# Kernel tuning notes

Hardware: AMD Instinct MI355X
Metric: run time of the kernel (lower is better)

## Reference

```python
import jax, jax.numpy as jnp
import numpy as np

B, N, L, D, O = 64, 4096, 64, 512, 7
K = 10  # topk neighbors per ligand atom (k=10 in pool_lig)
EPS_BN = 1e-5


def setup_inputs() -> dict:
    key = jax.random.key(0)
    ks = jax.random.split(key, 6)
    pos = jax.random.normal(ks[0], (B, N, 3), jnp.float32) * 10.0
    x = jax.random.normal(ks[1], (B, N, D), jnp.float32)
    lig_coords = jax.random.normal(ks[2], (B, L, 3), jnp.float32) * 10.0
    W1 = jax.random.normal(ks[3], (D, D), jnp.float32) / np.sqrt(D).astype(np.float32)
    b1 = jnp.zeros((D,), jnp.float32)
    gamma = jnp.ones((D,), jnp.float32)
    beta = jnp.zeros((D,), jnp.float32)
    W2 = jax.random.normal(ks[4], (O, D), jnp.float32) / np.sqrt(D).astype(np.float32)
    b2 = jnp.zeros((O,), jnp.float32)
    return dict(pos=pos, x=x, lig_coords=lig_coords, W1=W1, b1=b1,
                gamma=gamma, beta=beta, W2=W2, b2=b2)


def _pool_lig(pos_b, x_b, lig_b):
    # cdist: [N, L] pairwise euclidean distances
    d = jnp.sqrt(jnp.sum((pos_b[:, None, :] - lig_b[None, :, :]) ** 2, axis=-1))
    # topk(-d, k=K, dim=0): K nearest surface points per ligand atom -> [L, K]
    idx = jax.lax.top_k(-d.T, K)[1]
    # .unique() + gather + mean == mean over the set of unique selected rows.
    # Implement via a 0/1 membership mask (scatter-set dedups repeats).
    mask = jnp.zeros((pos_b.shape[0],), x_b.dtype).at[idx.reshape(-1)].set(1.0)
    return (mask[:, None] * x_b).sum(axis=0) / mask.sum()  # [D]


def reference(pos, x, lig_coords, W1, b1, gamma, beta, W2, b2):
    emb = jax.vmap(_pool_lig)(pos, x, lig_coords)  # [B, D]
    h = emb @ W1.T + b1                             # Linear(D, D)
    # Dropout(p=0.1): identity (eval / deterministic reference)
    mu = h.mean(axis=0)
    var = h.var(axis=0)  # biased variance, as BatchNorm1d (training stats)
    h = gamma * (h - mu) / jnp.sqrt(var + EPS_BN) + beta
    h = h * jax.nn.sigmoid(h)                       # SiLU
    return h @ W2.T + b2                            # [B, O]
```

## Files before the change

kernel.cpp:

```cpp
#include <hip/hip_runtime.h>

#define BATCH 64
#define NPTS  4096
#define LIG   64
#define DIM   512
#define OUTF  7
#define TOPK  10

using ull = unsigned long long;

__device__ __forceinline__ ull shfl_down_u64(ull v, int off) {
    unsigned int lo = (unsigned int)v, hi = (unsigned int)(v >> 32);
    lo = __shfl_down(lo, off);
    hi = __shfl_down(hi, off);
    return ((ull)hi << 32) | lo;
}

__device__ __forceinline__ float dot4(float4 a, float4 b) {
    return a.x * b.x + a.y * b.y + a.z * b.z + a.w * b.w;
}

__global__ __launch_bounds__(256) void k_topk(
    const float* __restrict__ pos,
    const float* __restrict__ lig,
    int* __restrict__ idxbuf) {
    const int l = blockIdx.x;
    const int b = blockIdx.y;
    const int t = threadIdx.x;

    const float* lp = lig + ((size_t)b * LIG + l) * 3;
    const float lx = lp[0], ly = lp[1], lz = lp[2];

    const float4* src = (const float4*)(pos + (size_t)b * NPTS * 3) + t * 12;
    float w[48];
#pragma unroll
    for (int q = 0; q < 12; ++q) {
        float4 v = src[q];
        w[4 * q] = v.x; w[4 * q + 1] = v.y; w[4 * q + 2] = v.z; w[4 * q + 3] = v.w;
    }

    ull key[16];
#pragma unroll
    for (int i = 0; i < 16; ++i) {
        float dx = w[3 * i]     - lx;
        float dy = w[3 * i + 1] - ly;
        float dz = w[3 * i + 2] - lz;
        float d2 = dx * dx + dy * dy + dz * dz;
        key[i] = ((ull)__float_as_uint(d2) << 32) | (unsigned)(t * 16 + i);
    }

    __shared__ ull red[4];
    __shared__ unsigned int widx_sh;
    const int wave = t >> 6, lane = t & 63;

    for (int r = 0; r < TOPK; ++r) {
        ull k = key[0];
#pragma unroll
        for (int i = 1; i < 16; ++i) k = (key[i] < k) ? key[i] : k;
#pragma unroll
        for (int off = 32; off > 0; off >>= 1) {
            ull o = shfl_down_u64(k, off);
            k = (o < k) ? o : k;
        }
        if (lane == 0) red[wave] = k;
        __syncthreads();
        if (t == 0) {
            ull m = red[0];
#pragma unroll
            for (int i = 1; i < 4; ++i) m = (red[i] < m) ? red[i] : m;
            unsigned int widx = (unsigned int)m;
            widx_sh = widx;
            idxbuf[((size_t)b * LIG + l) * TOPK + r] = (int)widx;
        }
        __syncthreads();
        const unsigned int widx = widx_sh;
#pragma unroll
        for (int i = 0; i < 16; ++i)
            if (widx == (unsigned)(t * 16 + i)) key[i] = ~0ull;
    }
}

__global__ __launch_bounds__(256) void k_pool(
    const int* __restrict__ idxbuf,
    const float* __restrict__ x,
    float* __restrict__ emb) {
    const int c = blockIdx.x;
    const int b = blockIdx.y;
    const int t = threadIdx.x;

    __shared__ unsigned mword[NPTS / 32];
    __shared__ int list[LIG * TOPK];
    __shared__ int cnt;
    if (t == 0) cnt = 0;
    for (int i = t; i < NPTS / 32; i += 256) mword[i] = 0u;
    __syncthreads();

    const int* ib = idxbuf + (size_t)b * LIG * TOPK;
    for (int j = t; j < LIG * TOPK; j += 256) {
        int idx = ib[j];
        unsigned bit = 1u << (idx & 31);
        unsigned old = atomicOr(&mword[idx >> 5], bit);
        if (!(old & bit)) list[atomicAdd(&cnt, 1)] = idx;
    }
    __syncthreads();
    const int n_sel = cnt;
    const float inv = 1.0f / (float)n_sel;

    const float* xb = x + (size_t)b * NPTS * DIM + c * 256 + t;
    float a = 0.f;
    int j = 0;
    for (; j + 4 <= n_sel; j += 4) {
        int n0 = list[j], n1 = list[j + 1], n2 = list[j + 2], n3 = list[j + 3];
        float v0 = xb[(size_t)n0 * DIM];
        float v1 = xb[(size_t)n1 * DIM];
        float v2 = xb[(size_t)n2 * DIM];
        float v3 = xb[(size_t)n3 * DIM];
        a += v0 + v1 + v2 + v3;
    }
    for (; j < n_sel; ++j) a += xb[(size_t)list[j] * DIM];

    emb[(size_t)b * DIM + c * 256 + t] = a * inv;
}

__global__ __launch_bounds__(256) void k_fc1(
    const float* __restrict__ emb,
    const float* __restrict__ W1,
    const float* __restrict__ b1,
    float* __restrict__ h) {
    const int jc = blockIdx.x;
    const int b  = blockIdx.y;
    const int t  = threadIdx.x;
    const int wave = t >> 6, lane = t & 63;

    const float4* ep = (const float4*)(emb + (size_t)b * DIM) + lane * 2;
    float4 e0 = ep[0], e1 = ep[1];

#pragma unroll
    for (int q = 0; q < 16; ++q) {
        const int jj = jc * 64 + wave * 16 + q;
        const float4* wp = (const float4*)(W1 + (size_t)jj * DIM) + lane * 2;
        float s = dot4(wp[0], e0) + dot4(wp[1], e1);
#pragma unroll
        for (int off = 32; off > 0; off >>= 1) s += __shfl_down(s, off);
        if (lane == 0) h[(size_t)b * DIM + jj] = s + b1[jj];
    }
}

__global__ __launch_bounds__(512) void k_bn(
    const float* __restrict__ h,
    const float* __restrict__ gamma,
    const float* __restrict__ beta,
    float* __restrict__ hs) {
    const int jf = threadIdx.x;
    float s = 0.f, ss = 0.f;
#pragma unroll 8
    for (int b = 0; b < BATCH; ++b) {
        float v = h[(size_t)b * DIM + jf];
        s += v; ss += v * v;
    }
    const float mu  = s * (1.0f / BATCH);
    const float var = ss * (1.0f / BATCH) - mu * mu;
    const float inv = rsqrtf(var + 1e-5f);
    const float g  = gamma[jf];
    const float be = beta[jf];
#pragma unroll 8
    for (int b = 0; b < BATCH; ++b) {
        float v = h[(size_t)b * DIM + jf];
        float u = g * (v - mu) * inv + be;
        hs[(size_t)b * DIM + jf] = u / (1.0f + __expf(-u));
    }
}

__global__ __launch_bounds__(64) void k_fc2(
    const float* __restrict__ hs,
    const float* __restrict__ W2,
    const float* __restrict__ b2,
    float* __restrict__ out) {
    const int b = blockIdx.x;
    const int lane = threadIdx.x;
    const float4* hp = (const float4*)(hs + (size_t)b * DIM) + lane * 2;
    float4 h0 = hp[0], h1 = hp[1];
#pragma unroll
    for (int o = 0; o < OUTF; ++o) {
        const float4* wp = (const float4*)(W2 + (size_t)o * DIM) + lane * 2;
        float s = dot4(wp[0], h0) + dot4(wp[1], h1);
#pragma unroll
        for (int off = 32; off > 0; off >>= 1) s += __shfl_down(s, off);
        if (lane == 0) out[(size_t)b * OUTF + o] = s + b2[o];
    }
}

extern "C" void kernel_launch(void* const* d_in, const int* in_sizes, int n_in,
                              void* d_out, int out_size, void* d_ws, size_t ws_size,
                              hipStream_t stream) {
    const float* pos   = (const float*)d_in[0];
    const float* x     = (const float*)d_in[1];
    const float* lig   = (const float*)d_in[2];
    const float* W1    = (const float*)d_in[3];
    const float* b1    = (const float*)d_in[4];
    const float* gamma = (const float*)d_in[5];
    const float* beta  = (const float*)d_in[6];
    const float* W2    = (const float*)d_in[7];
    const float* b2    = (const float*)d_in[8];
    float* out = (float*)d_out;

    char* ws = (char*)d_ws;
    int*   idxbuf = (int*)ws;
    float* emb    = (float*)(ws + (size_t)BATCH * LIG * TOPK * 4);
    float* h      = emb + BATCH * DIM;
    float* hs     = h + BATCH * DIM;

    k_topk<<<dim3(LIG, BATCH), 256, 0, stream>>>(pos, lig, idxbuf);
    k_pool<<<dim3(2, BATCH), 256, 0, stream>>>(idxbuf, x, emb);
    k_fc1 <<<dim3(8, BATCH), 256, 0, stream>>>(emb, W1, b1, h);
    k_bn  <<<1, 512, 0, stream>>>(h, gamma, beta, hs);
    k_fc2 <<<BATCH, 64, 0, stream>>>(hs, W2, b2, out);
}
```

Measured before the change: 687.0 us.

## Split pooling gather across row-partition blocks and cache per-thread min in top-k

The pooling kernel now partitions the selected rows by index modulo 8 across 8 blocks per batch, not splitting columns across 2 blocks. Each block writes partial sums, and fc1 reduces them and divides by a popcount-based unique count. This raises parallelism for the latency-bound gather at the cost of extra partial traffic and a dedup pass repeated in every block. The top-k loop caches each thread's minimum and recomputes it only in the thread that owns the winner, and it uses double-buffered shared slots so one barrier per round suffices.

```diff
diff --git a/kernel.cpp b/kernel.cpp
--- a/kernel.cpp
+++ b/kernel.cpp
@@ -6,6 +6,7 @@
 #define DIM   512
 #define OUTF  7
 #define TOPK  10
+#define PBLK  8
 
 using ull = unsigned long long;
 
@@ -15,6 +16,8 @@
     hi = __shfl_down(hi, off);
     return ((ull)hi << 32) | lo;
 }
+
+__device__ __forceinline__ ull umin64(ull a, ull b) { return (a < b) ? a : b; }
 
 __device__ __forceinline__ float dot4(float4 a, float4 b) {
     return a.x * b.x + a.y * b.y + a.z * b.z + a.w * b.w;
@@ -49,49 +52,50 @@
         key[i] = ((ull)__float_as_uint(d2) << 32) | (unsigned)(t * 16 + i);
     }
 
-    __shared__ ull red[4];
-    __shared__ unsigned int widx_sh;
+    ull m = key[0];
+#pragma unroll
+    for (int i = 1; i < 16; ++i) m = umin64(m, key[i]);
+
+    __shared__ ull red[2][4];
     const int wave = t >> 6, lane = t & 63;
+    int* ob = idxbuf + ((size_t)b * LIG + l) * TOPK;
 
     for (int r = 0; r < TOPK; ++r) {
-        ull k = key[0];
-#pragma unroll
-        for (int i = 1; i < 16; ++i) k = (key[i] < k) ? key[i] : k;
-#pragma unroll
-        for (int off = 32; off > 0; off >>= 1) {
-            ull o = shfl_down_u64(k, off);
-            k = (o < k) ? o : k;
+        ull k = m;
+#pragma unroll
+        for (int off = 32; off > 0; off >>= 1)
+            k = umin64(k, shfl_down_u64(k, off));
+        if (lane == 0) red[r & 1][wave] = k;
+        __syncthreads();
+        const ull g = umin64(umin64(red[r & 1][0], red[r & 1][1]),
+                             umin64(red[r & 1][2], red[r & 1][3]));
+        const unsigned widx = (unsigned)g;
+        if (t == 0) ob[r] = (int)widx;
+        if ((widx >> 4) == (unsigned)t) {
+#pragma unroll
+            for (int i = 0; i < 16; ++i)
+                key[i] = (key[i] == g) ? ~0ull : key[i];
+            m = key[0];
+#pragma unroll
+            for (int i = 1; i < 16; ++i) m = umin64(m, key[i]);
         }
-        if (lane == 0) red[wave] = k;
-        __syncthreads();
-        if (t == 0) {
-            ull m = red[0];
-#pragma unroll
-            for (int i = 1; i < 4; ++i) m = (red[i] < m) ? red[i] : m;
-            unsigned int widx = (unsigned int)m;
-            widx_sh = widx;
-            idxbuf[((size_t)b * LIG + l) * TOPK + r] = (int)widx;
-        }
-        __syncthreads();
-        const unsigned int widx = widx_sh;
-#pragma unroll
-        for (int i = 0; i < 16; ++i)
-            if (widx == (unsigned)(t * 16 + i)) key[i] = ~0ull;
     }
 }
 
 __global__ __launch_bounds__(256) void k_pool(
     const int* __restrict__ idxbuf,
     const float* __restrict__ x,
-    float* __restrict__ emb) {
-    const int c = blockIdx.x;
+    float* __restrict__ partial,
+    int* __restrict__ nsel) {
+    const int p = blockIdx.x;
     const int b = blockIdx.y;
     const int t = threadIdx.x;
 
     __shared__ unsigned mword[NPTS / 32];
     __shared__ int list[LIG * TOPK];
     __shared__ int cnt;
-    if (t == 0) cnt = 0;
+    __shared__ int tot;
+    if (t == 0) { cnt = 0; tot = 0; }
     for (int i = t; i < NPTS / 32; i += 256) mword[i] = 0u;
     __syncthreads();
 
@@ -100,30 +104,47 @@
         int idx = ib[j];
         unsigned bit = 1u << (idx & 31);
         unsigned old = atomicOr(&mword[idx >> 5], bit);
-        if (!(old & bit)) list[atomicAdd(&cnt, 1)] = idx;
+        if (!(old & bit) && ((idx & 7) == p)) list[atomicAdd(&cnt, 1)] = idx;
     }
     __syncthreads();
-    const int n_sel = cnt;
-    const float inv = 1.0f / (float)n_sel;
-
-    const float* xb = x + (size_t)b * NPTS * DIM + c * 256 + t;
-    float a = 0.f;
+
+    int v = (t < NPTS / 32) ? (int)__popc(mword[t]) : 0;
+#pragma unroll
+    for (int off = 32; off > 0; off >>= 1) v += __shfl_down(v, off);
+    if ((t & 63) == 0) atomicAdd(&tot, v);
+    __syncthreads();
+    if (p == 0 && t == 0) nsel[b] = tot;
+
+    const int cn = cnt;
+    const float* xb = x + (size_t)b * NPTS * DIM + t;
+    float a0 = 0.f, a1 = 0.f;
     int j = 0;
-    for (; j + 4 <= n_sel; j += 4) {
+    for (; j + 3 < cn; j += 4) {
         int n0 = list[j], n1 = list[j + 1], n2 = list[j + 2], n3 = list[j + 3];
-        float v0 = xb[(size_t)n0 * DIM];
-        float v1 = xb[(size_t)n1 * DIM];
-        float v2 = xb[(size_t)n2 * DIM];
-        float v3 = xb[(size_t)n3 * DIM];
-        a += v0 + v1 + v2 + v3;
-    }
-    for (; j < n_sel; ++j) a += xb[(size_t)list[j] * DIM];
-
-    emb[(size_t)b * DIM + c * 256 + t] = a * inv;
+        const float* r0 = xb + (size_t)n0 * DIM;
+        const float* r1 = xb + (size_t)n1 * DIM;
+        const float* r2 = xb + (size_t)n2 * DIM;
+        const float* r3 = xb + (size_t)n3 * DIM;
+        float v00 = r0[0], v01 = r0[256];
+        float v10 = r1[0], v11 = r1[256];
+        float v20 = r2[0], v21 = r2[256];
+        float v30 = r3[0], v31 = r3[256];
+        a0 += v00 + v10 + v20 + v30;
+        a1 += v01 + v11 + v21 + v31;
+    }
+    for (; j < cn; ++j) {
+        const float* r0 = xb + (size_t)list[j] * DIM;
+        a0 += r0[0]; a1 += r0[256];
+    }
+
+    float* pb = partial + ((size_t)b * PBLK + p) * DIM;
+    pb[t] = a0;
+    pb[t + 256] = a1;
 }
 
 __global__ __launch_bounds__(256) void k_fc1(
-    const float* __restrict__ emb,
+    const float* __restrict__ partial,
+    const int* __restrict__ nsel,
     const float* __restrict__ W1,
     const float* __restrict__ b1,
     float* __restrict__ h) {
@@ -132,8 +153,17 @@
     const int t  = threadIdx.x;
     const int wave = t >> 6, lane = t & 63;
 
-    const float4* ep = (const float4*)(emb + (size_t)b * DIM) + lane * 2;
-    float4 e0 = ep[0], e1 = ep[1];
+    const float4* pp = (const float4*)(partial + (size_t)b * PBLK * DIM) + lane * 2;
+    float4 e0 = pp[0], e1 = pp[1];
+#pragma unroll
+    for (int r = 1; r < PBLK; ++r) {
+        float4 u0 = pp[r * (DIM / 4)], u1 = pp[r * (DIM / 4) + 1];
+        e0.x += u0.x; e0.y += u0.y; e0.z += u0.z; e0.w += u0.w;
+        e1.x += u1.x; e1.y += u1.y; e1.z += u1.z; e1.w += u1.w;
+    }
+    const float inv = 1.0f / (float)nsel[b];
+    e0.x *= inv; e0.y *= inv; e0.z *= inv; e0.w *= inv;
+    e1.x *= inv; e1.y *= inv; e1.z *= inv; e1.w *= inv;
 
 #pragma unroll
     for (int q = 0; q < 16; ++q) {
@@ -205,14 +235,15 @@
     float* out = (float*)d_out;
 
     char* ws = (char*)d_ws;
-    int*   idxbuf = (int*)ws;
-    float* emb    = (float*)(ws + (size_t)BATCH * LIG * TOPK * 4);
-    float* h      = emb + BATCH * DIM;
-    float* hs     = h + BATCH * DIM;
+    int*   idxbuf  = (int*)ws;
+    float* partial = (float*)(ws + (size_t)BATCH * LIG * TOPK * 4);
+    int*   nsel    = (int*)((char*)partial + (size_t)BATCH * PBLK * DIM * 4);
+    float* h       = (float*)((char*)nsel + 256);
+    float* hs      = h + BATCH * DIM;
 
     k_topk<<<dim3(LIG, BATCH), 256, 0, stream>>>(pos, lig, idxbuf);
-    k_pool<<<dim3(2, BATCH), 256, 0, stream>>>(idxbuf, x, emb);
-    k_fc1 <<<dim3(8, BATCH), 256, 0, stream>>>(emb, W1, b1, h);
+    k_pool<<<dim3(PBLK, BATCH), 256, 0, stream>>>(idxbuf, x, partial, nsel);
+    k_fc1 <<<dim3(8, BATCH), 256, 0, stream>>>(partial, nsel, W1, b1, h);
     k_bn  <<<1, 512, 0, stream>>>(h, gamma, beta, hs);
     k_fc2 <<<BATCH, 64, 0, stream>>>(hs, W2, b2, out);
 }
```

Result: faster. 670.1 us (-2.5%).
